# Kernel tuning notes

Measured on AMD Instinct MI355X. Metric: run time of the kernel, lower is better.

## Reference

```python
import jax, jax.numpy as jnp
import numpy as np

V = 50000   # input_size == output_size (one-hot vocab)
H = 256     # hidden_size
B = 512     # batch_size
L = 1       # num_layers

def setup_inputs() -> dict:
    key = jax.random.key(0)
    ks = jax.random.split(key, 9)
    s = 1.0 / np.sqrt(H)  # torch default uniform(-1/sqrt(H), 1/sqrt(H))
    inp = {
        "input": jax.random.randint(ks[0], (B,), 0, V, dtype=jnp.int64 if jax.config.jax_enable_x64 else jnp.int32),
        "target": jax.random.randint(ks[1], (B,), 0, V, dtype=jnp.int64 if jax.config.jax_enable_x64 else jnp.int32),
        "hidden": jax.random.normal(ks[2], (L, B, H), dtype=jnp.float32),
        "w_ih": jax.random.uniform(ks[3], (3 * H, V), jnp.float32, -s, s),
        "w_hh": jax.random.uniform(ks[4], (3 * H, H), jnp.float32, -s, s),
        "b_ih": jax.random.uniform(ks[5], (3 * H,), jnp.float32, -s, s),
        "b_hh": jax.random.uniform(ks[6], (3 * H,), jnp.float32, -s, s),
        "w_out": jax.random.uniform(ks[7], (V, H), jnp.float32, -s, s),
        "b_out": jax.random.uniform(ks[8], (V,), jnp.float32, -s, s),
    }
    return inp

def reference(input, target, hidden, w_ih, w_hh, b_ih, b_hh, w_out, b_out):
    # one-hot(input) @ w_ih.T is exactly a row-gather from w_ih.T  -> (B, 3H)
    h0 = hidden[0]                              # (B, H), num_layers == 1
    x_proj = w_ih.T[input] + b_ih               # (B, 3H)
    h_proj = h0 @ w_hh.T + b_hh                 # (B, 3H)
    xr, xz, xn = jnp.split(x_proj, 3, axis=-1)
    hr, hz, hn = jnp.split(h_proj, 3, axis=-1)
    r = jax.nn.sigmoid(xr + hr)                 # reset gate
    z = jax.nn.sigmoid(xz + hz)                 # update gate
    n = jnp.tanh(xn + r * hn)                   # candidate
    h1 = (1.0 - z) * n + z * h0                 # (B, H)
    logit = jnp.tanh(h1 @ w_out.T + b_out)      # (B, V)
    return logit, h1[None]                      # (B,V), (1,B,H)
```

## Files before the change

### kernel.cpp

```cpp
#include <hip/hip_runtime.h>
#include <hip/hip_bf16.h>

#define VOCAB 50000
#define HID   256
#define BATCH 512
#define GH    768

typedef __attribute__((ext_vector_type(8))) __bf16 bf16x8;
typedef __attribute__((ext_vector_type(4))) float f32x4;
typedef __attribute__((ext_vector_type(4))) unsigned int u32x4;

union BFrag {
    bf16x8 v;
    u32x4  q;
    unsigned short u[8];
};

__device__ __forceinline__ unsigned short f2bf(float f) {
    unsigned int x = __builtin_bit_cast(unsigned int, f);
    x += 0x7FFFu + ((x >> 16) & 1u);
    return (unsigned short)(x >> 16);
}

__device__ __forceinline__ float fast_sigmoid(float x) {
    return 1.0f / (1.0f + __expf(-x));
}
__device__ __forceinline__ float fast_tanh(float x) {
    return 1.0f - 2.0f / (1.0f + __expf(2.0f * x));
}

__device__ __forceinline__ void cvt8(BFrag& t, f32x4 lo, f32x4 hi) {
    t.u[0] = f2bf(lo.x); t.u[1] = f2bf(lo.y);
    t.u[2] = f2bf(lo.z); t.u[3] = f2bf(lo.w);
    t.u[4] = f2bf(hi.x); t.u[5] = f2bf(hi.y);
    t.u[6] = f2bf(hi.z); t.u[7] = f2bf(hi.w);
}


__global__ __launch_bounds__(256) void repack_f32(
    const float* __restrict__ src, u32x4* __restrict__ dst, int nFrag)
{
    int fid = blockIdx.x * 256 + threadIdx.x;
    if (fid >= nFrag) return;
    int r = fid & 15, g = (fid >> 4) & 3, kk = (fid >> 6) & 7, mt = fid >> 9;
    const f32x4* p = reinterpret_cast<const f32x4*>(
        src + (size_t)(mt * 16 + r) * 256 + kk * 32 + g * 8);
    BFrag t; cvt8(t, p[0], p[1]);
    dst[fid] = t.q;
}

template <int EPI>
__global__ __launch_bounds__(256, 2) void gemm_ms(
    const u32x4* __restrict__ Af, const float* __restrict__ Bm,
    float* __restrict__ C, const float* __restrict__ bias,
    int Ncols, int mChunks)
{
    const int tid  = threadIdx.x;
    const int wid  = tid >> 6;
    const int wr   = wid >> 1;
    const int wc   = wid & 1;
    const int lane = tid & 63;
    const int r    = lane & 15;
    const int g    = lane >> 4;
    const int colbase = blockIdx.x * 64 + wc * 32;

    BFrag bf[2][8];
    float biasv[2] = {0.f, 0.f};
    #pragma unroll
    for (int n = 0; n < 2; n++) {
        int col  = colbase + n * 16 + r;
        int bcol = col < Ncols ? col : (Ncols - 1);
        const f32x4* wrow = reinterpret_cast<const f32x4*>(Bm + (size_t)bcol * 256);
        #pragma unroll
        for (int kk = 0; kk < 8; kk++)
            cvt8(bf[n][kk], wrow[kk * 8 + g * 2], wrow[kk * 8 + g * 2 + 1]);
        if (EPI == 1) biasv[n] = bias[bcol];
    }
    #pragma unroll
    for (int n = 0; n < 2; n++)
        #pragma unroll
        for (int kk = 0; kk < 8; kk++)
            asm volatile("" : "+v"(bf[n][kk].q));

    for (int c = 0; c < mChunks; c++) {
        const int chunk = blockIdx.y * mChunks + c;
        const int mt0   = chunk * 4 + wr * 2;
        const u32x4* a0 = Af + (size_t)mt0 * 8 * 64 + lane;

        f32x4 acc[2][2];
        #pragma unroll
        for (int m = 0; m < 2; m++) {
            acc[m][0] = (f32x4){0.f, 0.f, 0.f, 0.f};
            acc[m][1] = (f32x4){0.f, 0.f, 0.f, 0.f};
        }

        #pragma unroll
        for (int kk = 0; kk < 8; kk++) {
            BFrag a0f, a1f;
            a0f.q = a0[kk * 64];
            a1f.q = a0[(8 + kk) * 64];
            acc[0][0] = __builtin_amdgcn_mfma_f32_16x16x32_bf16(a0f.v, bf[0][kk].v, acc[0][0], 0, 0, 0);
            acc[0][1] = __builtin_amdgcn_mfma_f32_16x16x32_bf16(a0f.v, bf[1][kk].v, acc[0][1], 0, 0, 0);
            acc[1][0] = __builtin_amdgcn_mfma_f32_16x16x32_bf16(a1f.v, bf[0][kk].v, acc[1][0], 0, 0, 0);
            acc[1][1] = __builtin_amdgcn_mfma_f32_16x16x32_bf16(a1f.v, bf[1][kk].v, acc[1][1], 0, 0, 0);
        }

        const int rowbase = chunk * 64 + wr * 32 + g * 4;
        #pragma unroll
        for (int m = 0; m < 2; m++) {
            #pragma unroll
            for (int n = 0; n < 2; n++) {
                int col = colbase + n * 16 + r;
                if (col < Ncols) {
                    #pragma unroll
                    for (int j = 0; j < 4; j++) {
                        float v = acc[m][n][j];
                        if (EPI == 1) v = fast_tanh(v + biasv[n]);
                        C[(size_t)(rowbase + m * 16 + j) * Ncols + col] = v;
                    }
                }
            }
        }
    }
}

__global__ __launch_bounds__(256) void gru_gate(
    const int* __restrict__ inp, const float* __restrict__ hidden,
    const float* __restrict__ w_ih, const float* __restrict__ b_ih,
    const float* __restrict__ b_hh, const float* __restrict__ hproj,
    float* __restrict__ h1out, unsigned short* __restrict__ h1frag)
{
    const int b = blockIdx.x;
    const int k = threadIdx.x;
    const int c = inp[b];

    float xr = w_ih[(size_t)k * VOCAB + c]         + b_ih[k];
    float xz = w_ih[(size_t)(k + 256) * VOCAB + c] + b_ih[k + 256];
    float xn = w_ih[(size_t)(k + 512) * VOCAB + c] + b_ih[k + 512];

    float hr = hproj[b * GH + k]       + b_hh[k];
    float hz = hproj[b * GH + 256 + k] + b_hh[k + 256];
    float hn = hproj[b * GH + 512 + k] + b_hh[k + 512];

    float rg = fast_sigmoid(xr + hr);
    float zg = fast_sigmoid(xz + hz);
    float ng = fast_tanh(xn + rg * hn);
    float h0 = hidden[b * HID + k];
    float h1 = (1.0f - zg) * ng + zg * h0;

    h1out[b * HID + k] = h1;

    int mt = b >> 4, rr = b & 15;
    int kk = k >> 5, gg = (k >> 3) & 3, e = k & 7;
    size_t fid = (size_t)((mt * 8 + kk) * 4 + gg) * 16 + rr;
    h1frag[fid * 8 + e] = f2bf(h1);
}

extern "C" void kernel_launch(void* const* d_in, const int* in_sizes, int n_in,
                              void* d_out, int out_size, void* d_ws, size_t ws_size,
                              hipStream_t stream) {
    const int*   input  = (const int*)  d_in[0];
    const float* hidden = (const float*)d_in[2];
    const float* w_ih   = (const float*)d_in[3];
    const float* w_hh   = (const float*)d_in[4];
    const float* b_ih   = (const float*)d_in[5];
    const float* b_hh   = (const float*)d_in[6];
    const float* w_out  = (const float*)d_in[7];
    const float* b_out  = (const float*)d_in[8];

    float* logit = (float*)d_out;
    float* h1    = (float*)d_out + (size_t)BATCH * VOCAB;

    u32x4* hfrag  = (u32x4*)d_ws;
    u32x4* h1frag = (u32x4*)((char*)d_ws + 256 * 1024);
    float* hproj  = (float*)((char*)d_ws + 512 * 1024);

    const int nFrag = BATCH * HID / 8;

    repack_f32<<<nFrag / 256, 256, 0, stream>>>(hidden, hfrag, nFrag);

    dim3 g1(GH / 64, BATCH / 64);
    gemm_ms<0><<<g1, 256, 0, stream>>>(hfrag, w_hh, hproj, nullptr, GH, 1);

    gru_gate<<<BATCH, 256, 0, stream>>>(input, hidden, w_ih, b_ih, b_hh, hproj,
                                        h1, (unsigned short*)h1frag);

    dim3 g3((VOCAB + 63) / 64, 1);
    gemm_ms<1><<<g3, 256, 0, stream>>>(h1frag, w_out, logit, b_out, VOCAB, 8);
}
```

Before: 73.66 us.

## Restructure output GEMM tiling to 8-wave blocks over columns with row-split grid

Each block now runs 8 waves that each own 32 output columns, covering 256 columns per block, and all waves share the same rows. The grid is split along rows (4 slices of 128 rows for the logit GEMM, 16 slices for the hidden projection), so each wave converts its w_out columns to bf16 once and reuses them across 4 row-chunks instead of 8. The manual round-to-nearest bf16 conversion is replaced with native __bf16 casts, which may map to hardware convert instructions. Splitting rows across blocks means each w_out column is loaded and converted 4 times instead of once, trading extra weight traffic for more parallel blocks.

```diff
diff --git a/kernel.cpp b/kernel.cpp
--- a/kernel.cpp
+++ b/kernel.cpp
@@ -13,14 +13,8 @@
 union BFrag {
     bf16x8 v;
     u32x4  q;
-    unsigned short u[8];
+    __bf16 b[8];
 };
-
-__device__ __forceinline__ unsigned short f2bf(float f) {
-    unsigned int x = __builtin_bit_cast(unsigned int, f);
-    x += 0x7FFFu + ((x >> 16) & 1u);
-    return (unsigned short)(x >> 16);
-}
 
 __device__ __forceinline__ float fast_sigmoid(float x) {
     return 1.0f / (1.0f + __expf(-x));
@@ -30,10 +24,10 @@
 }
 
 __device__ __forceinline__ void cvt8(BFrag& t, f32x4 lo, f32x4 hi) {
-    t.u[0] = f2bf(lo.x); t.u[1] = f2bf(lo.y);
-    t.u[2] = f2bf(lo.z); t.u[3] = f2bf(lo.w);
-    t.u[4] = f2bf(hi.x); t.u[5] = f2bf(hi.y);
-    t.u[6] = f2bf(hi.z); t.u[7] = f2bf(hi.w);
+    t.b[0] = (__bf16)lo.x; t.b[1] = (__bf16)lo.y;
+    t.b[2] = (__bf16)lo.z; t.b[3] = (__bf16)lo.w;
+    t.b[4] = (__bf16)hi.x; t.b[5] = (__bf16)hi.y;
+    t.b[6] = (__bf16)hi.z; t.b[7] = (__bf16)hi.w;
 }
 
 
@@ -50,19 +44,17 @@
 }
 
 template <int EPI>
-__global__ __launch_bounds__(256, 2) void gemm_ms(
+__global__ __launch_bounds__(512, 2) void gemm_direct(
     const u32x4* __restrict__ Af, const float* __restrict__ Bm,
     float* __restrict__ C, const float* __restrict__ bias,
     int Ncols, int mChunks)
 {
     const int tid  = threadIdx.x;
     const int wid  = tid >> 6;
-    const int wr   = wid >> 1;
-    const int wc   = wid & 1;
     const int lane = tid & 63;
     const int r    = lane & 15;
     const int g    = lane >> 4;
-    const int colbase = blockIdx.x * 64 + wc * 32;
+    const int colbase = blockIdx.x * 256 + wid * 32;
 
     BFrag bf[2][8];
     float biasv[2] = {0.f, 0.f};
@@ -82,10 +74,12 @@
         for (int kk = 0; kk < 8; kk++)
             asm volatile("" : "+v"(bf[n][kk].q));
 
+    const int rows0 = blockIdx.y * (mChunks * 32);
+
     for (int c = 0; c < mChunks; c++) {
-        const int chunk = blockIdx.y * mChunks + c;
-        const int mt0   = chunk * 4 + wr * 2;
-        const u32x4* a0 = Af + (size_t)mt0 * 8 * 64 + lane;
+        const int mt0 = (rows0 >> 4) + c * 2;
+        const u32x4* a0 = Af + (size_t)(mt0 * 8) * 64 + lane;
+        const u32x4* a1 = Af + (size_t)((mt0 + 1) * 8) * 64 + lane;
 
         f32x4 acc[2][2];
         #pragma unroll
@@ -96,16 +90,16 @@
 
         #pragma unroll
         for (int kk = 0; kk < 8; kk++) {
-            BFrag a0f, a1f;
-            a0f.q = a0[kk * 64];
-            a1f.q = a0[(8 + kk) * 64];
-            acc[0][0] = __builtin_amdgcn_mfma_f32_16x16x32_bf16(a0f.v, bf[0][kk].v, acc[0][0], 0, 0, 0);
-            acc[0][1] = __builtin_amdgcn_mfma_f32_16x16x32_bf16(a0f.v, bf[1][kk].v, acc[0][1], 0, 0, 0);
-            acc[1][0] = __builtin_amdgcn_mfma_f32_16x16x32_bf16(a1f.v, bf[0][kk].v, acc[1][0], 0, 0, 0);
-            acc[1][1] = __builtin_amdgcn_mfma_f32_16x16x32_bf16(a1f.v, bf[1][kk].v, acc[1][1], 0, 0, 0);
+            BFrag af0, af1;
+            af0.q = a0[kk * 64];
+            af1.q = a1[kk * 64];
+            acc[0][0] = __builtin_amdgcn_mfma_f32_16x16x32_bf16(af0.v, bf[0][kk].v, acc[0][0], 0, 0, 0);
+            acc[0][1] = __builtin_amdgcn_mfma_f32_16x16x32_bf16(af0.v, bf[1][kk].v, acc[0][1], 0, 0, 0);
+            acc[1][0] = __builtin_amdgcn_mfma_f32_16x16x32_bf16(af1.v, bf[0][kk].v, acc[1][0], 0, 0, 0);
+            acc[1][1] = __builtin_amdgcn_mfma_f32_16x16x32_bf16(af1.v, bf[1][kk].v, acc[1][1], 0, 0, 0);
         }
 
-        const int rowbase = chunk * 64 + wr * 32 + g * 4;
+        const int rowb = rows0 + c * 32 + g * 4;
         #pragma unroll
         for (int m = 0; m < 2; m++) {
             #pragma unroll
@@ -116,7 +110,7 @@
                     for (int j = 0; j < 4; j++) {
                         float v = acc[m][n][j];
                         if (EPI == 1) v = fast_tanh(v + biasv[n]);
-                        C[(size_t)(rowbase + m * 16 + j) * Ncols + col] = v;
+                        C[(size_t)(rowb + m * 16 + j) * Ncols + col] = v;
                     }
                 }
             }
@@ -153,7 +147,8 @@
     int mt = b >> 4, rr = b & 15;
     int kk = k >> 5, gg = (k >> 3) & 3, e = k & 7;
     size_t fid = (size_t)((mt * 8 + kk) * 4 + gg) * 16 + rr;
-    h1frag[fid * 8 + e] = f2bf(h1);
+    __bf16 hb = (__bf16)h1;
+    h1frag[fid * 8 + e] = __builtin_bit_cast(unsigned short, hb);
 }
 
 extern "C" void kernel_launch(void* const* d_in, const int* in_sizes, int n_in,
@@ -179,12 +174,12 @@
 
     repack_f32<<<nFrag / 256, 256, 0, stream>>>(hidden, hfrag, nFrag);
 
-    dim3 g1(GH / 64, BATCH / 64);
-    gemm_ms<0><<<g1, 256, 0, stream>>>(hfrag, w_hh, hproj, nullptr, GH, 1);
+    dim3 g1((GH + 255) / 256, 16);
+    gemm_direct<0><<<g1, 512, 0, stream>>>(hfrag, w_hh, hproj, nullptr, GH, 1);
 
     gru_gate<<<BATCH, 256, 0, stream>>>(input, hidden, w_ih, b_ih, b_hh, hproj,
                                         h1, (unsigned short*)h1frag);
 
-    dim3 g3((VOCAB + 63) / 64, 1);
-    gemm_ms<1><<<g3, 256, 0, stream>>>(h1frag, w_out, logit, b_out, VOCAB, 8);
+    dim3 g3((VOCAB + 255) / 256, 4);
+    gemm_direct<1><<<g3, 512, 0, stream>>>(h1frag, w_out, logit, b_out, VOCAB, 4);
 }
```

Result: slower. 110.5 us (+50.1%).
